# Performance work log

Measured on AMD Instinct MI355X. Metric: run time of the kernel, lower is better.

Reference implementation:

```python
import jax, jax.numpy as jnp
import numpy as np

K = 9          # kernel_size
PAD = K // 2   # same padding
SIGMA = 1.0
EPS = 1e-5     # BatchNorm eps


def setup_inputs() -> dict:
    key = jax.random.key(0)
    k0, k1, k2 = jax.random.split(key, 3)
    B, Cin, Cout, L = 4, 64, 64, 131072
    x = jax.random.normal(k0, (B, Cin, L), jnp.float32)
    coords = jax.random.uniform(k1, (B, 3, L), jnp.float32)  # 3D point coords in [0,1)
    W = jax.random.normal(k2, (Cout, Cin, K), jnp.float32) * (1.0 / np.sqrt(Cin * K))
    bias = jnp.zeros((Cout,), jnp.float32)
    gamma = jnp.ones((Cout,), jnp.float32)
    beta = jnp.zeros((Cout,), jnp.float32)
    return {"x": x, "coords": coords, "W": W, "bias": bias, "gamma": gamma, "beta": beta}


def reference(x, coords, W, bias, gamma, beta):
    B, Cin, L = x.shape
    # zero-pad sequence dim for 'same' conv
    xpad = jnp.pad(x, ((0, 0), (0, 0), (PAD, PAD)))
    cpad = jnp.pad(coords, ((0, 0), (0, 0), (PAD, PAD)))
    # unfold: neighbor windows of size K (K is a small compile-time constant)
    x_unf = jnp.stack([xpad[:, :, k:k + L] for k in range(K)], axis=2)   # [B,Cin,K,L]
    c_unf = jnp.stack([cpad[:, :, k:k + L] for k in range(K)], axis=2)   # [B,3,K,L]
    # Gaussian spatial weights from coord distances (WeightedConv1D)
    dist2 = jnp.sum((c_unf - coords[:, :, None, :]) ** 2, axis=1)        # [B,K,L]
    w = jnp.exp(-dist2 / (2.0 * SIGMA * SIGMA))                          # [B,K,L]
    # weighted conv: contract over (Cin, K)
    out = jnp.einsum('ock,bckl->bol', W, x_unf * w[:, None, :, :])       # [B,Cout,L]
    out = out + bias[None, :, None]
    # BatchNorm1d (training-mode batch statistics over B and L) + ReLU
    mean = out.mean(axis=(0, 2), keepdims=True)
    var = out.var(axis=(0, 2), keepdims=True)
    out = (out - mean) * jax.lax.rsqrt(var + EPS)
    out = out * gamma[None, :, None] + beta[None, :, None]
    return jax.nn.relu(out)
```

## Files before the change

### kernel.cpp

```cpp
#include <hip/hip_runtime.h>
#include <hip/hip_bf16.h>

#define KK 9
#define PADK 4
#define CIN 64
#define COUT 64
#define LSEQ 131072
#define NB 4
#define TILE 64
#define XROWS 72
#define XRS 72
#define NTILES 2048
#define NPART 64

typedef __attribute__((ext_vector_type(8))) short v8s;
typedef __attribute__((ext_vector_type(4))) float v4f;

__device__ __forceinline__ unsigned short f2bf(float f) {
  __hip_bfloat16 h = __float2bfloat16(f);
  return *reinterpret_cast<unsigned short*>(&h);
}
__device__ __forceinline__ float bf2f(unsigned short s) {
  return __uint_as_float(((unsigned)s) << 16);
}

__device__ __forceinline__ void store_o(float* p, float v) { *p = v; }
__device__ __forceinline__ void store_o(__hip_bfloat16* p, float v) { *p = __float2bfloat16(v); }

__global__ void wtrans_kernel(const float* __restrict__ W, v8s* __restrict__ Wt) {
  int t = blockIdx.x * 256 + threadIdx.x;
  if (t >= KK * 2 * 4 * 64) return;
  int lane = t & 63;
  int frag = t >> 6;
  int mblk = frag & 3;
  int s    = (frag >> 2) & 1;
  int k    = frag >> 3;
  int m = lane & 15, q = lane >> 4;
  int o = mblk * 16 + m;
  union { v8s v; unsigned short h[8]; } u;
#pragma unroll
  for (int j = 0; j < 8; ++j) {
    int c = 32 * s + q * 8 + j;
    u.h[j] = f2bf(W[(o * CIN + c) * KK + k]);
  }
  Wt[t] = u.v;
}

template <typename OutT>
__global__ __launch_bounds__(64, 3)
void conv_kernel(const float* __restrict__ x, const float* __restrict__ coords,
                 const v8s* __restrict__ Wt, OutT* __restrict__ cv,
                 float* __restrict__ stat_sum, float* __restrict__ stat_sq) {
  __shared__ __align__(16) __hip_bfloat16 xt[XROWS][XRS];
  __shared__ float wt[KK][TILE];

  const int lane = threadIdx.x & 63;
  const int gw   = blockIdx.x;
  const int b    = gw >> 11;
  const int tile = gw & (NTILES - 1);
  const int l0   = tile * TILE;
  const float* xb = x + (b * CIN) * LSEQ;
  const float* cb = coords + (b * 3) * LSEQ;
  const int m = lane & 15;
  const int q = lane >> 4;

#pragma unroll
  for (int rep = 0; rep < 2; ++rep) {
    int cg = 8 * (q + 4 * rep);
    float4 f[8];
#pragma unroll
    for (int t = 0; t < 8; ++t)
      f[t] = *(const float4*)(xb + (cg + t) * LSEQ + l0 + 4 * m);
    const float* fp = (const float*)&f[0];
#pragma unroll
    for (int j = 0; j < 4; ++j) {
      union { v8s v; unsigned short h[8]; } u;
#pragma unroll
      for (int t = 0; t < 8; ++t) u.h[t] = f2bf(fp[4 * t + j]);
      *(v8s*)&xt[4 + 4 * m + j][cg] = u.v;
    }
  }
  {
    int c = lane;
    float el[4] = {0.f, 0.f, 0.f, 0.f};
    float er[4] = {0.f, 0.f, 0.f, 0.f};
    if (tile != 0) {
#pragma unroll
      for (int j = 0; j < 4; ++j) el[j] = xb[c * LSEQ + l0 - 4 + j];
    }
    if (tile != NTILES - 1) {
#pragma unroll
      for (int j = 0; j < 4; ++j) er[j] = xb[c * LSEQ + l0 + TILE + j];
    }
#pragma unroll
    for (int j = 0; j < 4; ++j) {
      xt[j][c]      = __float2bfloat16(el[j]);
      xt[68 + j][c] = __float2bfloat16(er[j]);
    }
  }
  {
    int n = lane;
    float sx = cb[l0 + n];
    float sy = cb[LSEQ + l0 + n];
    float sz = cb[2 * LSEQ + l0 + n];
    float w9[KK];
#pragma unroll
    for (int k = 0; k < KK; ++k) {
      int l = l0 + n + k - PADK;
      float cx = 0.f, cy = 0.f, cz = 0.f;
      if ((unsigned)l < (unsigned)LSEQ) {
        cx = cb[l]; cy = cb[LSEQ + l]; cz = cb[2 * LSEQ + l];
      }
      float dx = cx - sx, dy = cy - sy, dz = cz - sz;
      w9[k] = __expf(-0.5f * (dx * dx + dy * dy + dz * dz));
    }
#pragma unroll
    for (int k = 0; k < KK; ++k)
      wt[k][n] = w9[k] - ((k < KK - 1) ? w9[k + 1] : 0.f);
  }
  __syncthreads();

  v4f y[4][4], tot[4][4];
#pragma unroll
  for (int i = 0; i < 4; ++i)
#pragma unroll
    for (int j = 0; j < 4; ++j) {
      y[i][j]   = (v4f){0.f, 0.f, 0.f, 0.f};
      tot[i][j] = (v4f){0.f, 0.f, 0.f, 0.f};
    }

#pragma unroll 1
  for (int k = 0; k < KK; ++k) {
    const v8s* wk = Wt + k * 512;
#pragma unroll
    for (int s = 0; s < 2; ++s) {
      v8s a0 = wk[(s * 4 + 0) * 64 + lane];
      v8s a1 = wk[(s * 4 + 1) * 64 + lane];
      v8s a2 = wk[(s * 4 + 2) * 64 + lane];
      v8s a3 = wk[(s * 4 + 3) * 64 + lane];
#pragma unroll
      for (int nb = 0; nb < 4; ++nb) {
        v8s bf = *(const v8s*)&xt[nb * 16 + m + k][q * 8 + 32 * s];
        y[0][nb] = __builtin_amdgcn_mfma_f32_16x16x32_bf16(a0, bf, y[0][nb], 0, 0, 0);
        y[1][nb] = __builtin_amdgcn_mfma_f32_16x16x32_bf16(a1, bf, y[1][nb], 0, 0, 0);
        y[2][nb] = __builtin_amdgcn_mfma_f32_16x16x32_bf16(a2, bf, y[2][nb], 0, 0, 0);
        y[3][nb] = __builtin_amdgcn_mfma_f32_16x16x32_bf16(a3, bf, y[3][nb], 0, 0, 0);
      }
    }
#pragma unroll
    for (int nb = 0; nb < 4; ++nb) {
      float d = wt[k][nb * 16 + m];
#pragma unroll
      for (int mb = 0; mb < 4; ++mb)
#pragma unroll
        for (int r = 0; r < 4; ++r)
          tot[mb][nb][r] = __builtin_fmaf(d, y[mb][nb][r], tot[mb][nb][r]);
    }
  }

  const int part = gw & (NPART - 1);
  OutT* outb = cv + (b * COUT) * LSEQ;
#pragma unroll
  for (int mb = 0; mb < 4; ++mb) {
#pragma unroll
    for (int r = 0; r < 4; ++r) {
      int o = mb * 16 + q * 4 + r;
      float s1 = 0.f, s2 = 0.f;
#pragma unroll
      for (int nb = 0; nb < 4; ++nb) {
        float v = tot[mb][nb][r];
        s1 += v;
        s2 += v * v;
        store_o(&outb[o * LSEQ + l0 + nb * 16 + m], v);
      }
#pragma unroll
      for (int off = 1; off < 16; off <<= 1) {
        s1 += __shfl_xor(s1, off, 64);
        s2 += __shfl_xor(s2, off, 64);
      }
      if (m == 0) {
        atomicAdd(&stat_sum[part * COUT + o], s1);
        atomicAdd(&stat_sq [part * COUT + o], s2);
      }
    }
  }
}

__global__ void finalize_kernel(const float* __restrict__ stat_sum,
                                const float* __restrict__ stat_sq,
                                const float* __restrict__ gamma,
                                const float* __restrict__ beta,
                                float* __restrict__ ss) {
  int o = threadIdx.x;
  float s1 = 0.f, s2 = 0.f;
  for (int p = 0; p < NPART; ++p) {
    s1 += stat_sum[p * COUT + o];
    s2 += stat_sq [p * COUT + o];
  }
  const float invN = 1.0f / (float)(NB * LSEQ);
  float mean = s1 * invN;
  float var  = s2 * invN - mean * mean;
  float sc = gamma[o] * rsqrtf(var + 1e-5f);
  ss[o]        = sc;
  ss[COUT + o] = beta[o] - mean * sc;
}

__global__ __launch_bounds__(256)
void scale_f32_kernel(float* __restrict__ data, const float* __restrict__ ss) {
  const int blk = blockIdx.x;
  const int ch = (blk >> 6) & 63;
  const float sc = ss[ch];
  const float sh = ss[COUT + ch];
  const int base = blk * 2048 + threadIdx.x * 8;
  float4 a = *(float4*)(data + base);
  float4 b = *(float4*)(data + base + 4);
  a.x = fmaxf(fmaf(a.x, sc, sh), 0.f);
  a.y = fmaxf(fmaf(a.y, sc, sh), 0.f);
  a.z = fmaxf(fmaf(a.z, sc, sh), 0.f);
  a.w = fmaxf(fmaf(a.w, sc, sh), 0.f);
  b.x = fmaxf(fmaf(b.x, sc, sh), 0.f);
  b.y = fmaxf(fmaf(b.y, sc, sh), 0.f);
  b.z = fmaxf(fmaf(b.z, sc, sh), 0.f);
  b.w = fmaxf(fmaf(b.w, sc, sh), 0.f);
  *(float4*)(data + base)     = a;
  *(float4*)(data + base + 4) = b;
}

__global__ __launch_bounds__(256)
void scale_bf16_kernel(const __hip_bfloat16* __restrict__ cvin,
                       const float* __restrict__ ss, float* __restrict__ out) {
  const int blk = blockIdx.x;
  const int ch = (blk >> 6) & 63;
  const float sc = ss[ch];
  const float sh = ss[COUT + ch];
  const int base = blk * 2048 + threadIdx.x * 8;
  union { v8s v; unsigned short h[8]; } u;
  u.v = *(const v8s*)(cvin + base);
  float r[8];
#pragma unroll
  for (int i = 0; i < 8; ++i)
    r[i] = fmaxf(fmaf(bf2f(u.h[i]), sc, sh), 0.f);
  *(float4*)(out + base)     = make_float4(r[0], r[1], r[2], r[3]);
  *(float4*)(out + base + 4) = make_float4(r[4], r[5], r[6], r[7]);
}

extern "C" void kernel_launch(void* const* d_in, const int* in_sizes, int n_in,
                              void* d_out, int out_size, void* d_ws, size_t ws_size,
                              hipStream_t stream) {
  const float* x      = (const float*)d_in[0];
  const float* coords = (const float*)d_in[1];
  const float* W      = (const float*)d_in[2];
  const float* gamma  = (const float*)d_in[4];
  const float* beta   = (const float*)d_in[5];
  float* out = (float*)d_out;
  char* ws = (char*)d_ws;

  float* stat_sum = (float*)(ws);
  float* stat_sq  = (float*)(ws + 16384);
  float* ss       = (float*)(ws + 32768);
  v8s*   Wt       = (v8s*)(ws + 40960);
  __hip_bfloat16* scratch = (__hip_bfloat16*)(ws + 131072);

  const size_t need_bf16 = (size_t)131072 + (size_t)NB * COUT * LSEQ * 2;
  const bool bf16_path = ws_size >= need_bf16;

  hipMemsetAsync(ws, 0, 32768, stream);
  wtrans_kernel<<<18, 256, 0, stream>>>(W, Wt);

  if (bf16_path) {
    conv_kernel<__hip_bfloat16><<<NB * NTILES, 64, 0, stream>>>(
        x, coords, Wt, scratch, stat_sum, stat_sq);
    finalize_kernel<<<1, COUT, 0, stream>>>(stat_sum, stat_sq, gamma, beta, ss);
    scale_bf16_kernel<<<(NB * COUT * (LSEQ / 2048)), 256, 0, stream>>>(scratch, ss, out);
  } else {
    conv_kernel<float><<<NB * NTILES, 64, 0, stream>>>(
        x, coords, Wt, out, stat_sum, stat_sq);
    finalize_kernel<<<1, COUT, 0, stream>>>(stat_sum, stat_sq, gamma, beta, ss);
    scale_f32_kernel<<<(NB * COUT * (LSEQ / 2048)), 256, 0, stream>>>(out, ss);
  }
}
```

Baseline: 328.5 us.

## Split conv tile across four waves, one per output-channel block

The conv kernel moves from one 64-thread wave per tile to a 256-thread block of four waves. Each wave computes 16 output channels, so per-thread accumulators drop from 32 v4f to 8. The x tile load and halo fill are spread across all 256 threads, and each wave prefetches the next k's weight fragments during the loop. Per-wave register pressure falls and more waves can hide latency, at the cost of the Gaussian weight computation running on only one wave while the other three wait at the barrier.

```diff
diff --git a/kernel.cpp b/kernel.cpp
--- a/kernel.cpp
+++ b/kernel.cpp
@@ -47,14 +47,16 @@
 }
 
 template <typename OutT>
-__global__ __launch_bounds__(64, 3)
+__global__ __launch_bounds__(256, 5)
 void conv_kernel(const float* __restrict__ x, const float* __restrict__ coords,
                  const v8s* __restrict__ Wt, OutT* __restrict__ cv,
                  float* __restrict__ stat_sum, float* __restrict__ stat_sq) {
   __shared__ __align__(16) __hip_bfloat16 xt[XROWS][XRS];
   __shared__ float wt[KK][TILE];
 
-  const int lane = threadIdx.x & 63;
+  const int tid  = threadIdx.x;
+  const int wv   = tid >> 6;
+  const int lane = tid & 63;
   const int gw   = blockIdx.x;
   const int b    = gw >> 11;
   const int tile = gw & (NTILES - 1);
@@ -64,42 +66,45 @@
   const int m = lane & 15;
   const int q = lane >> 4;
 
-#pragma unroll
-  for (int rep = 0; rep < 2; ++rep) {
-    int cg = 8 * (q + 4 * rep);
-    float4 f[8];
-#pragma unroll
-    for (int t = 0; t < 8; ++t)
-      f[t] = *(const float4*)(xb + (cg + t) * LSEQ + l0 + 4 * m);
+  {
+    int mm = tid & 15;
+    int c4 = (tid >> 4) * 4;
+    float4 f[4];
+#pragma unroll
+    for (int t = 0; t < 4; ++t)
+      f[t] = *(const float4*)(xb + (c4 + t) * LSEQ + l0 + 4 * mm);
     const float* fp = (const float*)&f[0];
 #pragma unroll
     for (int j = 0; j < 4; ++j) {
-      union { v8s v; unsigned short h[8]; } u;
-#pragma unroll
-      for (int t = 0; t < 8; ++t) u.h[t] = f2bf(fp[4 * t + j]);
-      *(v8s*)&xt[4 + 4 * m + j][cg] = u.v;
-    }
-  }
-  {
-    int c = lane;
-    float el[4] = {0.f, 0.f, 0.f, 0.f};
-    float er[4] = {0.f, 0.f, 0.f, 0.f};
-    if (tile != 0) {
-#pragma unroll
-      for (int j = 0; j < 4; ++j) el[j] = xb[c * LSEQ + l0 - 4 + j];
-    }
-    if (tile != NTILES - 1) {
-#pragma unroll
-      for (int j = 0; j < 4; ++j) er[j] = xb[c * LSEQ + l0 + TILE + j];
-    }
-#pragma unroll
-    for (int j = 0; j < 4; ++j) {
-      xt[j][c]      = __float2bfloat16(el[j]);
-      xt[68 + j][c] = __float2bfloat16(er[j]);
-    }
-  }
-  {
-    int n = lane;
+      union { unsigned long long v; unsigned short h[4]; } u;
+#pragma unroll
+      for (int t = 0; t < 4; ++t) u.h[t] = f2bf(fp[4 * t + j]);
+      *(unsigned long long*)&xt[4 + 4 * mm + j][c4] = u.v;
+    }
+  }
+  if (tid < 128) {
+    int side = tid >> 6;
+    int c = tid & 63;
+    if (side == 0) {
+      float el[4] = {0.f, 0.f, 0.f, 0.f};
+      if (tile != 0) {
+#pragma unroll
+        for (int j = 0; j < 4; ++j) el[j] = xb[c * LSEQ + l0 - 4 + j];
+      }
+#pragma unroll
+      for (int j = 0; j < 4; ++j) xt[j][c] = __float2bfloat16(el[j]);
+    } else {
+      float er[4] = {0.f, 0.f, 0.f, 0.f};
+      if (tile != NTILES - 1) {
+#pragma unroll
+        for (int j = 0; j < 4; ++j) er[j] = xb[c * LSEQ + l0 + TILE + j];
+      }
+#pragma unroll
+      for (int j = 0; j < 4; ++j) xt[68 + j][c] = __float2bfloat16(er[j]);
+    }
+  }
+  if (tid < 64) {
+    int n = tid;
     float sx = cb[l0 + n];
     float sy = cb[LSEQ + l0 + n];
     float sz = cb[2 * LSEQ + l0 + n];
@@ -120,68 +125,60 @@
   }
   __syncthreads();
 
-  v4f y[4][4], tot[4][4];
-#pragma unroll
-  for (int i = 0; i < 4; ++i)
-#pragma unroll
-    for (int j = 0; j < 4; ++j) {
-      y[i][j]   = (v4f){0.f, 0.f, 0.f, 0.f};
-      tot[i][j] = (v4f){0.f, 0.f, 0.f, 0.f};
-    }
+  v4f y[4], tot[4];
+#pragma unroll
+  for (int j = 0; j < 4; ++j) {
+    y[j]   = (v4f){0.f, 0.f, 0.f, 0.f};
+    tot[j] = (v4f){0.f, 0.f, 0.f, 0.f};
+  }
+
+  const v8s* wp = Wt + wv * 64 + lane;
+  v8s a0 = wp[0];
+  v8s a1 = wp[256];
 
 #pragma unroll 1
   for (int k = 0; k < KK; ++k) {
-    const v8s* wk = Wt + k * 512;
-#pragma unroll
-    for (int s = 0; s < 2; ++s) {
-      v8s a0 = wk[(s * 4 + 0) * 64 + lane];
-      v8s a1 = wk[(s * 4 + 1) * 64 + lane];
-      v8s a2 = wk[(s * 4 + 2) * 64 + lane];
-      v8s a3 = wk[(s * 4 + 3) * 64 + lane];
-#pragma unroll
-      for (int nb = 0; nb < 4; ++nb) {
-        v8s bf = *(const v8s*)&xt[nb * 16 + m + k][q * 8 + 32 * s];
-        y[0][nb] = __builtin_amdgcn_mfma_f32_16x16x32_bf16(a0, bf, y[0][nb], 0, 0, 0);
-        y[1][nb] = __builtin_amdgcn_mfma_f32_16x16x32_bf16(a1, bf, y[1][nb], 0, 0, 0);
-        y[2][nb] = __builtin_amdgcn_mfma_f32_16x16x32_bf16(a2, bf, y[2][nb], 0, 0, 0);
-        y[3][nb] = __builtin_amdgcn_mfma_f32_16x16x32_bf16(a3, bf, y[3][nb], 0, 0, 0);
-      }
-    }
-#pragma unroll
-    for (int nb = 0; nb < 4; ++nb) {
-      float d = wt[k][nb * 16 + m];
-#pragma unroll
-      for (int mb = 0; mb < 4; ++mb)
-#pragma unroll
-        for (int r = 0; r < 4; ++r)
-          tot[mb][nb][r] = __builtin_fmaf(d, y[mb][nb][r], tot[mb][nb][r]);
+#pragma unroll
+    for (int nbq = 0; nbq < 4; ++nbq) {
+      const __hip_bfloat16* rowp = &xt[nbq * 16 + m + k][q * 8];
+      v8s b0 = *(const v8s*)(rowp);
+      v8s b1 = *(const v8s*)(rowp + 32);
+      y[nbq] = __builtin_amdgcn_mfma_f32_16x16x32_bf16(a0, b0, y[nbq], 0, 0, 0);
+      y[nbq] = __builtin_amdgcn_mfma_f32_16x16x32_bf16(a1, b1, y[nbq], 0, 0, 0);
+    }
+    int kn = k + (k < KK - 1);
+    a0 = wp[kn * 512];
+    a1 = wp[kn * 512 + 256];
+#pragma unroll
+    for (int nbq = 0; nbq < 4; ++nbq) {
+      float d = wt[k][nbq * 16 + m];
+#pragma unroll
+      for (int r = 0; r < 4; ++r)
+        tot[nbq][r] = __builtin_fmaf(d, y[nbq][r], tot[nbq][r]);
     }
   }
 
   const int part = gw & (NPART - 1);
   OutT* outb = cv + (b * COUT) * LSEQ;
 #pragma unroll
-  for (int mb = 0; mb < 4; ++mb) {
-#pragma unroll
-    for (int r = 0; r < 4; ++r) {
-      int o = mb * 16 + q * 4 + r;
-      float s1 = 0.f, s2 = 0.f;
-#pragma unroll
-      for (int nb = 0; nb < 4; ++nb) {
-        float v = tot[mb][nb][r];
-        s1 += v;
-        s2 += v * v;
-        store_o(&outb[o * LSEQ + l0 + nb * 16 + m], v);
-      }
-#pragma unroll
-      for (int off = 1; off < 16; off <<= 1) {
-        s1 += __shfl_xor(s1, off, 64);
-        s2 += __shfl_xor(s2, off, 64);
-      }
-      if (m == 0) {
-        atomicAdd(&stat_sum[part * COUT + o], s1);
-        atomicAdd(&stat_sq [part * COUT + o], s2);
-      }
+  for (int r = 0; r < 4; ++r) {
+    int o = wv * 16 + q * 4 + r;
+    float s1 = 0.f, s2 = 0.f;
+#pragma unroll
+    for (int nbq = 0; nbq < 4; ++nbq) {
+      float v = tot[nbq][r];
+      s1 += v;
+      s2 += v * v;
+      store_o(&outb[o * LSEQ + l0 + nbq * 16 + m], v);
+    }
+#pragma unroll
+    for (int off = 1; off < 16; off <<= 1) {
+      s1 += __shfl_xor(s1, off, 64);
+      s2 += __shfl_xor(s2, off, 64);
+    }
+    if (m == 0) {
+      atomicAdd(&stat_sum[part * COUT + o], s1);
+      atomicAdd(&stat_sq [part * COUT + o], s2);
     }
   }
 }
@@ -268,12 +265,12 @@
   wtrans_kernel<<<18, 256, 0, stream>>>(W, Wt);
 
   if (bf16_path) {
-    conv_kernel<__hip_bfloat16><<<NB * NTILES, 64, 0, stream>>>(
+    conv_kernel<__hip_bfloat16><<<NB * NTILES, 256, 0, stream>>>(
         x, coords, Wt, scratch, stat_sum, stat_sq);
     finalize_kernel<<<1, COUT, 0, stream>>>(stat_sum, stat_sq, gamma, beta, ss);
     scale_bf16_kernel<<<(NB * COUT * (LSEQ / 2048)), 256, 0, stream>>>(scratch, ss, out);
   } else {
-    conv_kernel<float><<<NB * NTILES, 64, 0, stream>>>(
+    conv_kernel<float><<<NB * NTILES, 256, 0, stream>>>(
         x, coords, Wt, out, stat_sum, stat_sq);
     finalize_kernel<<<1, COUT, 0, stream>>>(stat_sum, stat_sq, gamma, beta, ss);
     scale_f32_kernel<<<(NB * COUT * (LSEQ / 2048)), 256, 0, stream>>>(out, ss);
```

Measured after the change: 322.6 us. Within noise of the previous version (-1.8%).
